# Optimization experiments

Hardware: AMD Instinct MI355X
Metric: run time of the kernel (lower is better)

## Reference

```python
import jax, jax.numpy as jnp
import numpy as np

B, N, D, H, DEPTH = 2, 2048, 768, 12, 4
DH = D // H
SCALE = DH ** -0.5
EPS = 1e-5
FF = 4 * D


def layer_norm(x, w, b):
    m = jnp.mean(x, axis=-1, keepdims=True)
    v = jnp.mean((x - m) ** 2, axis=-1, keepdims=True)
    return (x - m) * jax.lax.rsqrt(v + EPS) * w + b


def to_heads(t):  # [b, n, D] -> [b, H, n, DH]
    b, n, _ = t.shape
    return t.reshape(b, n, H, DH).transpose(0, 2, 1, 3)


def merge_heads(t):  # [b, H, n, DH] -> [b, n, D]
    b, h, n, dh = t.shape
    return t.transpose(0, 2, 1, 3).reshape(b, n, D)


def attend(q, k, v, bias):
    s = jnp.einsum('bhid,bhjd->bhij', q, k) * SCALE + bias
    a = jax.nn.softmax(s, axis=-1)
    return merge_heads(jnp.einsum('bhij,bhjd->bhid', a, v))


def setup_inputs():
    key = jax.random.key(0)
    ks = iter(jax.random.split(key, 16))

    def p(shape, scale=0.02):
        return jax.random.normal(next(ks), shape, dtype=jnp.float32) * scale

    inp = {
        'x': jax.random.normal(next(ks), (B, N, D), dtype=jnp.float32),
        'context': jax.random.normal(next(ks), (B, N, D), dtype=jnp.float32),
        'relative_position_bias': jax.random.normal(next(ks), (1, H, N, N), dtype=jnp.float32) * 0.02,
        # self-attn params (stacked over depth)
        'ln1_w': jnp.ones((DEPTH, D), jnp.float32), 'ln1_b': jnp.zeros((DEPTH, D), jnp.float32),
        'w_qkv': p((DEPTH, D, 3 * D)),
        'w_so': p((DEPTH, D, D)), 'b_so': jnp.zeros((DEPTH, D), jnp.float32),
        # cross-attn params (shared LN applied to x and context, as in source)
        'ln2_w': jnp.ones((DEPTH, D), jnp.float32), 'ln2_b': jnp.zeros((DEPTH, D), jnp.float32),
        'w_q': p((DEPTH, D, D)), 'w_k': p((DEPTH, D, D)), 'w_v': p((DEPTH, D, D)),
        'w_co': p((DEPTH, D, D)), 'b_co': jnp.zeros((DEPTH, D), jnp.float32),
        # FFN params
        'ln3_w': jnp.ones((DEPTH, D), jnp.float32), 'ln3_b': jnp.zeros((DEPTH, D), jnp.float32),
        'w_f1': p((DEPTH, D, FF)), 'b_f1': jnp.zeros((DEPTH, FF), jnp.float32),
        'w_f2': p((DEPTH, FF, D)), 'b_f2': jnp.zeros((DEPTH, D), jnp.float32),
        # final norm
        'lnout_w': jnp.ones((D,), jnp.float32), 'lnout_b': jnp.zeros((D,), jnp.float32),
    }
    return inp


def reference(x, context, relative_position_bias,
              ln1_w, ln1_b, w_qkv, w_so, b_so,
              ln2_w, ln2_b, w_q, w_k, w_v, w_co, b_co,
              ln3_w, ln3_b, w_f1, b_f1, w_f2, b_f2,
              lnout_w, lnout_b):
    bias = relative_position_bias
    for i in range(DEPTH):
        # self-attention block (pre-norm, residual)
        xn = layer_norm(x, ln1_w[i], ln1_b[i])
        q, k, v = jnp.split(xn @ w_qkv[i], 3, axis=-1)
        o = attend(to_heads(q), to_heads(k), to_heads(v), bias)
        x = o @ w_so[i] + b_so[i] + x
        # cross-attention block (input_norm shared for x and context)
        xn = layer_norm(x, ln2_w[i], ln2_b[i])
        cn = layer_norm(context, ln2_w[i], ln2_b[i])
        o = attend(to_heads(xn @ w_q[i]), to_heads(cn @ w_k[i]), to_heads(cn @ w_v[i]), bias)
        x = o @ w_co[i] + b_co[i] + x
        # FFN block
        xn = layer_norm(x, ln3_w[i], ln3_b[i])
        h = jax.nn.gelu(xn @ w_f1[i] + b_f1[i], approximate=False)
        x = h @ w_f2[i] + b_f2[i] + x
    return layer_norm(x, lnout_w, lnout_b)
```

## Files before the change

kernel.cpp:

```cpp
#include <hip/hip_runtime.h>
#include <cstdint>
#include <cstddef>

#define DEV static __device__ __forceinline__

typedef float  f32x4 __attribute__((ext_vector_type(4)));
typedef float  f32x2 __attribute__((ext_vector_type(2)));
typedef short  s16x8 __attribute__((ext_vector_type(8)));
typedef unsigned short u16;
typedef unsigned int   u32;
typedef unsigned int   u32x4 __attribute__((ext_vector_type(4)));
typedef unsigned short u16x2 __attribute__((ext_vector_type(2)));
typedef unsigned short u16x4 __attribute__((ext_vector_type(4)));
typedef __bf16 bf16x8 __attribute__((ext_vector_type(8)));

#define LOG2E 1.4426950408889634f
#define QSCALE_CONST 0.18033688011112042f
#define BSCALE 256.0f
#define BINV   0.00390625f

DEV u16 f2bf(float f){ return __builtin_bit_cast(u16, (__bf16)f); }

DEV float fexp2(float x){
#if __has_builtin(__builtin_amdgcn_exp2f)
  return __builtin_amdgcn_exp2f(x);
#else
  return exp2f(x);
#endif
}

DEV f32x4 mfma16(s16x8 a, s16x8 b, f32x4 c){
  return __builtin_amdgcn_mfma_f32_16x16x32_bf16(
      __builtin_bit_cast(bf16x8, a), __builtin_bit_cast(bf16x8, b), c, 0, 0, 0);
}

DEV void gld16(const void* g, void* l){
  __builtin_amdgcn_global_load_lds(
      (const __attribute__((address_space(1))) void*)(uintptr_t)g,
      (__attribute__((address_space(3))) void*)(unsigned)(uintptr_t)l,
      16, 0, 0);
}

#if __has_builtin(__builtin_amdgcn_cvt_pk_fp8_f32) && __has_builtin(__builtin_amdgcn_cvt_pk_f32_fp8)
DEV u32 pk4_fp8(f32x4 v){
  int r = __builtin_amdgcn_cvt_pk_fp8_f32(v[0], v[1], 0, false);
  r     = __builtin_amdgcn_cvt_pk_fp8_f32(v[2], v[3], r, true);
  return (u32)r;
}
template<bool HI>
DEV f32x2 upk_fp8(u32 w){
  return __builtin_amdgcn_cvt_pk_f32_fp8((int)w, HI);
}
#else
DEV unsigned enc1(float x){
  union{float f; unsigned u;} c; c.f = x;
  unsigned s = (c.u >> 24) & 0x80;
  int e = (int)((c.u >> 23) & 0xff) - 127;
  unsigned m = c.u & 0x7fffff;
  if (e >= -6){
    unsigned mant = m >> 20, rem = m & 0xfffff;
    if (rem > 0x80000 || (rem == 0x80000 && (mant & 1))) mant++;
    unsigned eb = (unsigned)(e + 7);
    if (mant == 8){ mant = 0; eb++; }
    if (eb >= 16){ eb = 15; mant = 6; }
    return s | (eb << 3) | mant;
  }
  if (e < -10) return s;
  int sh = -6 - e;
  unsigned full = (1u << 23) | m;
  unsigned mant = full >> (20 + sh);
  unsigned rem  = full & ((1u << (20 + sh)) - 1);
  unsigned half = 1u << (19 + sh);
  if (rem > half || (rem == half && (mant & 1))) mant++;
  if (mant == 8) return s | (1u << 3);
  return s | mant;
}
DEV u32 pk4_fp8(f32x4 v){
  return enc1(v[0]) | (enc1(v[1]) << 8) | (enc1(v[2]) << 16) | (enc1(v[3]) << 24);
}
DEV float dec1(unsigned b){
  int s = (b >> 7) & 1, e = (b >> 3) & 15; float m = (float)(b & 7) * 0.125f;
  float v = e ? ldexpf(1.0f + m, e - 7) : ldexpf(m, -6);
  return s ? -v : v;
}
template<bool HI>
DEV f32x2 upk_fp8(u32 w){
  unsigned lo = HI ? ((w >> 16) & 0xff) : (w & 0xff);
  unsigned h2 = HI ? ((w >> 24) & 0xff) : ((w >> 8) & 0xff);
  f32x2 r; r[0] = dec1(lo); r[1] = dec1(h2); return r;
}
#endif

__global__ void __launch_bounds__(256)
transpose_cvt(const float* __restrict__ src, u16* __restrict__ dst, int K, int N,
              size_t dzstride){
  int z = blockIdx.z;
  src += (size_t)z * K * N;
  dst += (size_t)z * dzstride;
  __shared__ float t[32][33];
  int n0 = blockIdx.x * 32, k0 = blockIdx.y * 32;
#pragma unroll
  for (int i = 0; i < 4; ++i)
    t[threadIdx.y + 8*i][threadIdx.x] = src[(size_t)(k0 + threadIdx.y + 8*i) * N + n0 + threadIdx.x];
  __syncthreads();
#pragma unroll
  for (int i = 0; i < 4; ++i)
    dst[(size_t)(n0 + threadIdx.y + 8*i) * K + k0 + threadIdx.x] = f2bf(t[threadIdx.x][threadIdx.y + 8*i]);
}

__global__ void __launch_bounds__(256)
cvt_biasT(const float* __restrict__ in, unsigned char* __restrict__ out){
  const int kvt = blockIdx.x, qt = blockIdx.y, h = blockIdx.z, tid = threadIdx.x;
  const int q  = qt * 64 + ((tid >> 6) << 4) + (tid & 15);
  const int c0 = kvt * 64 + ((tid >> 4) & 3) * 4;
  const float* src = in + ((size_t)h * 2048 + q) * 2048;
  u32x4 wv;
#pragma unroll
  for (int mi = 0; mi < 4; ++mi){
    f32x4 v = *(const f32x4*)(src + c0 + mi * 16);
#pragma unroll
    for (int r = 0; r < 4; ++r) v[r] = fminf(fmaxf(v[r] * (LOG2E * BSCALE), -448.f), 448.f);
    wv[mi] = pk4_fp8(v);
  }
  *(u32x4*)(out + ((size_t)(h * 32 + qt) * 32 + kvt) * 4096 + tid * 16) = wv;
}

__global__ void __launch_bounds__(256)
lnv(const float* __restrict__ x, const float* __restrict__ w, const float* __restrict__ b,
    u16* __restrict__ out){
  const int wv = threadIdx.x >> 6, lane = threadIdx.x & 63;
  const float* wz = w + blockIdx.y * 768;
  const float* bz = b + blockIdx.y * 768;
  out += (size_t)blockIdx.y * 4096 * 768;
  const int row = blockIdx.x * 4 + wv;
  const float* xr = x + (size_t)row * 768;
  f32x4 t[3]; float s = 0.f, s2 = 0.f;
#pragma unroll
  for (int c = 0; c < 3; ++c){
    t[c] = *(const f32x4*)(xr + c * 256 + lane * 4);
#pragma unroll
    for (int j = 0; j < 4; ++j){ s += t[c][j]; s2 += t[c][j] * t[c][j]; }
  }
#pragma unroll
  for (int off = 1; off < 64; off <<= 1){ s += __shfl_xor(s, off); s2 += __shfl_xor(s2, off); }
  float m = s * (1.f/768.f);
  float rstd = rsqrtf(s2 * (1.f/768.f) - m * m + 1e-5f);
#pragma unroll
  for (int c = 0; c < 3; ++c){
    const int col = c * 256 + lane * 4;
    f32x4 wv4 = *(const f32x4*)(wz + col);
    f32x4 bv4 = *(const f32x4*)(bz + col);
    u16x4 o;
#pragma unroll
    for (int j = 0; j < 4; ++j) o[j] = f2bf((t[c][j] - m) * rstd * wv4[j] + bv4[j]);
    *(u16x4*)(out + (size_t)row * 768 + col) = o;
  }
}

template<typename OUT>
__global__ void __launch_bounds__(256)
red_ln(const float* __restrict__ p, const float* __restrict__ biasrow,
       float* __restrict__ xbuf, OUT* __restrict__ out,
       const float* __restrict__ lw, const float* __restrict__ lb){
  const int wv = threadIdx.x >> 6, lane = threadIdx.x & 63;
  const int row = blockIdx.x * 4 + wv;
  const size_t S = 4096ll * 768;
  const float* p0 = p + (size_t)row * 768;
  float* xr = xbuf + (size_t)row * 768;
  f32x4 t[3]; float s = 0.f, s2 = 0.f;
#pragma unroll
  for (int c = 0; c < 3; ++c){
    const int col = c * 256 + lane * 4;
    f32x4 v = *(const f32x4*)(p0 + col);
    v += *(const f32x4*)(p0 + S + col);
    v += *(const f32x4*)(p0 + 2*S + col);
    v += *(const f32x4*)(p0 + 3*S + col);
    v += *(const f32x4*)(biasrow + col);
    v += *(const f32x4*)(xr + col);
    *(f32x4*)(xr + col) = v;
    t[c] = v;
#pragma unroll
    for (int j = 0; j < 4; ++j){ s += v[j]; s2 += v[j] * v[j]; }
  }
#pragma unroll
  for (int off = 1; off < 64; off <<= 1){ s += __shfl_xor(s, off); s2 += __shfl_xor(s2, off); }
  float m = s * (1.f/768.f);
  float rstd = rsqrtf(s2 * (1.f/768.f) - m * m + 1e-5f);
#pragma unroll
  for (int c = 0; c < 3; ++c){
    const int col = c * 256 + lane * 4;
    f32x4 wv4 = *(const f32x4*)(lw + col);
    f32x4 bv4 = *(const f32x4*)(lb + col);
    if constexpr (sizeof(OUT) == 2){
      u16x4 o;
#pragma unroll
      for (int j = 0; j < 4; ++j) o[j] = f2bf((t[c][j] - m) * rstd * wv4[j] + bv4[j]);
      *(u16x4*)((u16*)out + (size_t)row * 768 + col) = o;
    } else {
      f32x4 o;
#pragma unroll
      for (int j = 0; j < 4; ++j) o[j] = (t[c][j] - m) * rstd * wv4[j] + bv4[j];
      *(f32x4*)((float*)out + (size_t)row * 768 + col) = o;
    }
  }
}

template<int EPI>
__global__ void __launch_bounds__(256)
gemm_bf16(const u16* __restrict__ A, int lda, const u16* __restrict__ Bt, int ldb,
          int nk, u16* __restrict__ Cb, float* __restrict__ Cf, int ldc,
          const float* __restrict__ bias,
          const u16* __restrict__ A2, const u16* __restrict__ Bt2){
  __shared__ u16 As[2][128 * 32];
  __shared__ u16 Bs[2][128 * 32];
  float colscale = 1.0f;
  if constexpr (EPI == 4){
    const int z = blockIdx.z;
    if (z == 0){ colscale = QSCALE_CONST; }
    else { A = A2; Bt = Bt2 + (size_t)(z - 1) * 768 * 768; }
    Cb += z * 768;
  }
  if constexpr (EPI == 5){
    const int z = blockIdx.z;
    A  += (size_t)z * nk * 32;
    Bt += (size_t)z * nk * 32;
    Cf += (size_t)z * 4096 * 768;
  }
  const int tid = threadIdx.x, w = tid >> 6, lane = tid & 63;
  const int l16 = lane & 15, g = lane >> 4;
  const int m0 = blockIdx.x * 128, n0 = blockIdx.y * 128;
  const int wm = (w >> 1) * 64, wn = (w & 1) * 64;
  f32x4 acc[4][4] = {};

  const u16* a0 = A  + (size_t)(m0 + (tid >> 2)) * lda + (tid & 3) * 8;
  const u16* a1 = A  + (size_t)(m0 + (tid >> 2) + 64) * lda + (tid & 3) * 8;
  const u16* b0 = Bt + (size_t)(n0 + (tid >> 2)) * ldb + (tid & 3) * 8;
  const u16* b1 = Bt + (size_t)(n0 + (tid >> 2) + 64) * ldb + (tid & 3) * 8;

  {
    char* ab = (char*)As[0]; char* bb = (char*)Bs[0];
    gld16(a0, ab + w * 1024); gld16(a1, ab + 4096 + w * 1024);
    gld16(b0, bb + w * 1024); gld16(b1, bb + 4096 + w * 1024);
  }
  __syncthreads();

  int cb = 0;
  for (int kt = 0; kt < nk; ++kt){
    if (kt + 1 < nk){
      const int k1 = (kt + 1) * 32;
      char* ab = (char*)As[cb ^ 1]; char* bb = (char*)Bs[cb ^ 1];
      gld16(a0 + k1, ab + w * 1024); gld16(a1 + k1, ab + 4096 + w * 1024);
      gld16(b0 + k1, bb + w * 1024); gld16(b1 + k1, bb + 4096 + w * 1024);
    }
    const u16* Ab = As[cb]; const u16* Bb = Bs[cb];
    s16x8 af[4], bfv[4];
#pragma unroll
    for (int mi = 0; mi < 4; ++mi)
      af[mi] = *(const s16x8*)(Ab + (wm + mi*16 + l16) * 32 + 8 * g);
#pragma unroll
    for (int ni = 0; ni < 4; ++ni)
      bfv[ni] = *(const s16x8*)(Bb + (wn + ni*16 + l16) * 32 + 8 * g);
#pragma unroll
    for (int mi = 0; mi < 4; ++mi)
#pragma unroll
      for (int ni = 0; ni < 4; ++ni)
        acc[mi][ni] = mfma16(af[mi], bfv[ni], acc[mi][ni]);
    __syncthreads();
    cb ^= 1;
  }

#pragma unroll
  for (int mi = 0; mi < 4; ++mi){
    const int rg = m0 + wm + mi*16 + 4*g;
#pragma unroll
    for (int ni = 0; ni < 4; ++ni){
      const int col = n0 + wn + ni*16 + l16;
      f32x4 v = acc[mi][ni];
#pragma unroll
      for (int r = 0; r < 4; ++r){
        const int row = rg + r;
        if constexpr (EPI == 2){
          float t = v[r] + bias[col];
          float ge = 0.5f * t * (1.0f + erff(t * 0.7071067811865476f));
          Cb[(size_t)row * ldc + col] = f2bf(ge);
        } else if constexpr (EPI == 3){
          float sc = (col < 768) ? QSCALE_CONST : 1.0f;
          Cb[(size_t)row * ldc + col] = f2bf(v[r] * sc);
        } else if constexpr (EPI == 4){
          Cb[(size_t)row * ldc + col] = f2bf(v[r] * colscale);
        } else {
          Cf[(size_t)row * 768 + col] = v[r];
        }
      }
    }
  }
}

__global__ void __launch_bounds__(256)
attn_kernel(const u16* __restrict__ qkv, const unsigned char* __restrict__ biasT,
            u16* __restrict__ out){
  __shared__ __align__(16) u16 Ks[2][4096];
  __shared__ __align__(16) u16 Vt[2][4096];
  __shared__ __align__(16) u16 Pl[4][1024];

  const int tid = threadIdx.x, w = tid >> 6, lane = tid & 63;
  const int l16 = lane & 15, g = lane >> 4;
  const int qt = blockIdx.x, h = blockIdx.y, b = blockIdx.z;
  const int rowbase = b * 2048, q0 = qt * 64;

  const int ci0 = w * 64 + lane, ci1 = ci0 + 256;
  const int r0 = ci0 >> 3, sc0 = ci0 & 7, r1 = ci1 >> 3, sc1 = ci1 & 7;
  const u16* kp0 = qkv + (size_t)(rowbase + r0) * 2304 + 768 + h * 64 + (((sc0 ^ (r0 & 7)) & 7) << 3);
  const u16* kp1 = qkv + (size_t)(rowbase + r1) * 2304 + 768 + h * 64 + (((sc1 ^ (r1 & 7)) & 7) << 3);
  const int dh0 = (tid & 31) * 2, vs = tid >> 5;
  const u16* vp = qkv + (size_t)(rowbase + vs * 8) * 2304 + 1536 + h * 64 + dh0;
  u16x2 vr[8];
  const unsigned char* bT = biasT + ((size_t)(h * 32 + qt) * 32) * 4096 + tid * 16;
  u32x4 brW, bnW;

  const u16* qrow = qkv + (size_t)(rowbase + q0 + w * 16 + l16) * 2304 + h * 64;
  s16x8 qf0 = *(const s16x8*)(qrow + 8 * g);
  s16x8 qf1 = *(const s16x8*)(qrow + 32 + 8 * g);

  f32x4 oacc[4] = {};
  float mrun = -3.0e38f, lrun = 0.f;
  const int sw = l16 & 7;

  {
    char* kb = (char*)Ks[0] + w * 1024;
    gld16(kp0, kb); gld16(kp1, kb + 4096);
#pragma unroll
    for (int i = 0; i < 8; ++i) vr[i] = *(const u16x2*)(vp + (size_t)i * 2304);
    brW = *(const u32x4*)(bT);
    s16x8 vA, vB;
#pragma unroll
    for (int j = 0; j < 8; ++j){ vA[j] = (short)vr[j][0]; vB[j] = (short)vr[j][1]; }
    *(s16x8*)(Vt[0] + dh0 * 64 + ((vs ^ (dh0 & 7)) << 3)) = vA;
    *(s16x8*)(Vt[0] + (dh0 + 1) * 64 + ((vs ^ ((dh0 + 1) & 7)) << 3)) = vB;
  }
  __syncthreads();

  for (int t = 0; t < 32; ++t){
    const int cb = t & 1;
    if (t < 31){
      const size_t koff = (size_t)(t + 1) * 64 * 2304;
      char* kb = (char*)Ks[cb ^ 1] + w * 1024;
      gld16(kp0 + koff, kb); gld16(kp1 + koff, kb + 4096);
      const u16* p = vp + koff;
#pragma unroll
      for (int i = 0; i < 8; ++i) vr[i] = *(const u16x2*)(p + (size_t)i * 2304);
      bnW = *(const u32x4*)(bT + (size_t)(t + 1) * 4096);
    }

    f32x4 st[4];
    __builtin_amdgcn_s_setprio(1);
#pragma unroll
    for (int mi = 0; mi < 4; ++mi){
      const int row = l16 + 16 * mi;
      s16x8 kf0 = *(const s16x8*)(Ks[cb] + row * 64 + ((g ^ sw) << 3));
      s16x8 kf1 = *(const s16x8*)(Ks[cb] + row * 64 + (((g + 4) ^ sw) << 3));
      f32x4 z = {};
      z = mfma16(kf0, qf0, z);
      st[mi] = mfma16(kf1, qf1, z);
    }
    __builtin_amdgcn_s_setprio(0);

    float tmax = -3.0e38f;
#pragma unroll
    for (int mi = 0; mi < 4; ++mi){
      f32x2 lo = upk_fp8<false>(brW[mi]);
      f32x2 hi = upk_fp8<true>(brW[mi]);
      st[mi][0] = fmaf(lo[0], BINV, st[mi][0]);
      st[mi][1] = fmaf(lo[1], BINV, st[mi][1]);
      st[mi][2] = fmaf(hi[0], BINV, st[mi][2]);
      st[mi][3] = fmaf(hi[1], BINV, st[mi][3]);
#pragma unroll
      for (int r = 0; r < 4; ++r) tmax = fmaxf(tmax, st[mi][r]);
    }
    tmax = fmaxf(tmax, __shfl_xor(tmax, 16));
    tmax = fmaxf(tmax, __shfl_xor(tmax, 32));
    if (!__all(tmax <= mrun + 8.f)){
      float mnew = fmaxf(mrun, tmax);
      float al = fexp2(mrun - mnew);
      mrun = mnew;
      lrun *= al;
#pragma unroll
      for (int r = 0; r < 4; ++r){
        float aq = __shfl(al, 4 * g + r);
#pragma unroll
        for (int ni = 0; ni < 4; ++ni) oacc[ni][r] *= aq;
      }
    }
    float ssum = 0.f;
#pragma unroll
    for (int mi = 0; mi < 4; ++mi){
      u16x4 pk;
#pragma unroll
      for (int r = 0; r < 4; ++r){
        float pv = fexp2(st[mi][r] - mrun);
        ssum += pv;
        pk[r] = f2bf(pv);
      }
      *(u16x4*)(Pl[w] + l16 * 64 + (((2*mi + (g >> 1)) ^ sw) << 3) + 4 * (g & 1)) = pk;
    }
    ssum += __shfl_xor(ssum, 16);
    ssum += __shfl_xor(ssum, 32);
    lrun += ssum;

    __builtin_amdgcn_s_setprio(1);
#pragma unroll
    for (int ks2 = 0; ks2 < 2; ++ks2){
      s16x8 pf = *(const s16x8*)(Pl[w] + l16 * 64 + (((4*ks2 + g) ^ sw) << 3));
#pragma unroll
      for (int ni = 0; ni < 4; ++ni){
        const int dh = l16 + 16 * ni;
        s16x8 vf = *(const s16x8*)(Vt[cb] + dh * 64 + (((4*ks2 + g) ^ sw) << 3));
        oacc[ni] = mfma16(pf, vf, oacc[ni]);
      }
    }
    __builtin_amdgcn_s_setprio(0);

    if (t < 31){
      s16x8 vA, vB;
#pragma unroll
      for (int j = 0; j < 8; ++j){ vA[j] = (short)vr[j][0]; vB[j] = (short)vr[j][1]; }
      *(s16x8*)(Vt[cb ^ 1] + dh0 * 64 + ((vs ^ (dh0 & 7)) << 3)) = vA;
      *(s16x8*)(Vt[cb ^ 1] + (dh0 + 1) * 64 + ((vs ^ ((dh0 + 1) & 7)) << 3)) = vB;
      brW = bnW;
    }
    __syncthreads();
  }

#pragma unroll
  for (int r = 0; r < 4; ++r){
    float lq = __shfl(lrun, 4 * g + r);
    float inv = 1.0f / lq;
    const int row = rowbase + q0 + w * 16 + 4 * g + r;
#pragma unroll
    for (int ni = 0; ni < 4; ++ni)
      out[(size_t)row * 768 + h * 64 + l16 + 16 * ni] = f2bf(oacc[ni][r] * inv);
  }
}

extern "C" void kernel_launch(void* const* d_in, const int* in_sizes, int n_in,
                              void* d_out, int out_size, void* d_ws, size_t ws_size,
                              hipStream_t stream){
  const float* in_x    = (const float*)d_in[0];
  const float* in_ctx  = (const float*)d_in[1];
  const float* in_bias = (const float*)d_in[2];
  const float* ln1_w = (const float*)d_in[3];
  const float* ln1_b = (const float*)d_in[4];
  const float* w_qkv = (const float*)d_in[5];
  const float* w_so  = (const float*)d_in[6];
  const float* b_so  = (const float*)d_in[7];
  const float* ln2_w = (const float*)d_in[8];
  const float* ln2_b = (const float*)d_in[9];
  const float* w_q   = (const float*)d_in[10];
  const float* w_k   = (const float*)d_in[11];
  const float* w_v   = (const float*)d_in[12];
  const float* w_co  = (const float*)d_in[13];
  const float* b_co  = (const float*)d_in[14];
  const float* ln3_w = (const float*)d_in[15];
  const float* ln3_b = (const float*)d_in[16];
  const float* w_f1  = (const float*)d_in[17];
  const float* b_f1  = (const float*)d_in[18];
  const float* w_f2  = (const float*)d_in[19];
  const float* b_f2  = (const float*)d_in[20];
  const float* lnout_w = (const float*)d_in[21];
  const float* lnout_b = (const float*)d_in[22];

  char* p = (char*)d_ws;
  float* xbuf  = (float*)p;  p += 4096ll * 768 * 4;
  float* pbuf  = (float*)p;  p += 4ll * 4096 * 768 * 4;
  u16* xn      = (u16*)p;    p += 4096ll * 768 * 2;
  u16* cn      = (u16*)p;    p += 4ll * 4096 * 768 * 2;
  u16* qkvb    = (u16*)p;    p += 4096ll * 2304 * 2;
  u16* attO    = (u16*)p;    p += 4096ll * 768 * 2;
  u16* ffh     = (u16*)p;    p += 4096ll * 3072 * 2;
  u16* wqkvT   = (u16*)p;    p += 4ll * 2304 * 768 * 2;
  u16* wsoT    = (u16*)p;    p += 4ll * 768 * 768 * 2;
  u16* wqT     = (u16*)p;    p += 4ll * 768 * 768 * 2;
  u16* wkvT    = (u16*)p;    p += 4ll * 1536 * 768 * 2;
  u16* wcoT    = (u16*)p;    p += 4ll * 768 * 768 * 2;
  u16* wf1T    = (u16*)p;    p += 4ll * 3072 * 768 * 2;
  u16* wf2T    = (u16*)p;    p += 4ll * 768 * 3072 * 2;
  unsigned char* biasT = (unsigned char*)p; p += 12ll * 2048 * 2048;

  hipMemcpyAsync(xbuf, in_x, 4096ll * 768 * 4, hipMemcpyDeviceToDevice, stream);

  const dim3 tb(32, 8);
  transpose_cvt<<<dim3(72, 24, 4), tb, 0, stream>>>(w_qkv, wqkvT, 768, 2304, 2304ll*768);
  transpose_cvt<<<dim3(24, 24, 4), tb, 0, stream>>>(w_so,  wsoT,  768, 768,  768ll*768);
  transpose_cvt<<<dim3(24, 24, 4), tb, 0, stream>>>(w_q,   wqT,   768, 768,  768ll*768);
  transpose_cvt<<<dim3(24, 24, 4), tb, 0, stream>>>(w_k,   wkvT,             768, 768, 1536ll*768);
  transpose_cvt<<<dim3(24, 24, 4), tb, 0, stream>>>(w_v,   wkvT + 768ll*768, 768, 768, 1536ll*768);
  transpose_cvt<<<dim3(24, 24, 4), tb, 0, stream>>>(w_co,  wcoT,  768, 768,  768ll*768);
  transpose_cvt<<<dim3(96, 24, 4), tb, 0, stream>>>(w_f1,  wf1T,  768, 3072, 3072ll*768);
  transpose_cvt<<<dim3(24, 96, 4), tb, 0, stream>>>(w_f2,  wf2T,  3072, 768, 768ll*3072);
  cvt_biasT<<<dim3(32, 32, 12), 256, 0, stream>>>(in_bias, biasT);
  lnv<<<dim3(1024, 4), 256, 0, stream>>>(in_ctx, ln2_w, ln2_b, cn);
  lnv<<<dim3(1024, 1), 256, 0, stream>>>(xbuf, ln1_w, ln1_b, xn);

  const dim3 ag(32, 12, 2);
  for (int i = 0; i < 4; ++i){
    gemm_bf16<3><<<dim3(32, 18), 256, 0, stream>>>(xn, 768, wqkvT + (size_t)i*2304*768, 768, 24,
                                                   qkvb, nullptr, 2304, nullptr, nullptr, nullptr);
    attn_kernel<<<ag, 256, 0, stream>>>(qkvb, biasT, attO);
    gemm_bf16<5><<<dim3(32, 6, 4), 256, 0, stream>>>(attO, 768, wsoT + (size_t)i*768*768, 768, 6,
                                                     nullptr, pbuf, 768, nullptr, nullptr, nullptr);
    red_ln<u16><<<1024, 256, 0, stream>>>(pbuf, b_so + i*768, xbuf, xn, ln2_w + i*768, ln2_b + i*768);
    gemm_bf16<4><<<dim3(32, 6, 3), 256, 0, stream>>>(xn, 768, wqT + (size_t)i*768*768, 768, 24,
                                                     qkvb, nullptr, 2304, nullptr,
                                                     cn + (size_t)i*4096*768, wkvT + (size_t)i*1536*768);
    attn_kernel<<<ag, 256, 0, stream>>>(qkvb, biasT, attO);
    gemm_bf16<5><<<dim3(32, 6, 4), 256, 0, stream>>>(attO, 768, wcoT + (size_t)i*768*768, 768, 6,
                                                     nullptr, pbuf, 768, nullptr, nullptr, nullptr);
    red_ln<u16><<<1024, 256, 0, stream>>>(pbuf, b_co + i*768, xbuf, xn, ln3_w + i*768, ln3_b + i*768);
    gemm_bf16<2><<<dim3(32, 24), 256, 0, stream>>>(xn, 768, wf1T + (size_t)i*3072*768, 768, 24,
                                                   ffh, nullptr, 3072, b_f1 + i*3072, nullptr, nullptr);
    gemm_bf16<5><<<dim3(32, 6, 4), 256, 0, stream>>>(ffh, 3072, wf2T + (size_t)i*768*3072, 3072, 24,
                                                     nullptr, pbuf, 768, nullptr, nullptr, nullptr);
    if (i < 3)
      red_ln<u16><<<1024, 256, 0, stream>>>(pbuf, b_f2 + i*768, xbuf, xn, ln1_w + (i+1)*768, ln1_b + (i+1)*768);
    else
      red_ln<float><<<1024, 256, 0, stream>>>(pbuf, b_f2 + i*768, xbuf, (float*)d_out, lnout_w, lnout_b);
  }
}
```

Before: 1.355 ms.

## Store split-K partials in bf16, remap GEMM blocks across XCDs, batch weight transposes

```diff
diff --git a/kernel.cpp b/kernel.cpp
--- a/kernel.cpp
+++ b/kernel.cpp
@@ -20,6 +20,7 @@
 #define BINV   0.00390625f
 
 DEV u16 f2bf(float f){ return __builtin_bit_cast(u16, (__bf16)f); }
+DEV float bf2f(u16 v){ union { unsigned u; float f; } x; x.u = ((unsigned)v) << 16; return x.f; }
 
 DEV float fexp2(float x){
 #if __has_builtin(__builtin_amdgcn_exp2f)
@@ -108,6 +109,22 @@
     dst[(size_t)(n0 + threadIdx.y + 8*i) * K + k0 + threadIdx.x] = f2bf(t[threadIdx.x][threadIdx.y + 8*i]);
 }
 
+struct TPtrs { const float* src[20]; u16* dst[20]; };
+__global__ void __launch_bounds__(256)
+transpose_cvt_batch(TPtrs tp){
+  const float* src = tp.src[blockIdx.z];
+  u16* dst = tp.dst[blockIdx.z];
+  __shared__ float t[32][33];
+  int n0 = blockIdx.x * 32, k0 = blockIdx.y * 32;
+#pragma unroll
+  for (int i = 0; i < 4; ++i)
+    t[threadIdx.y + 8*i][threadIdx.x] = src[(size_t)(k0 + threadIdx.y + 8*i) * 768 + n0 + threadIdx.x];
+  __syncthreads();
+#pragma unroll
+  for (int i = 0; i < 4; ++i)
+    dst[(size_t)(n0 + threadIdx.y + 8*i) * 768 + k0 + threadIdx.x] = f2bf(t[threadIdx.x][threadIdx.y + 8*i]);
+}
+
 __global__ void __launch_bounds__(256)
 cvt_biasT(const float* __restrict__ in, unsigned char* __restrict__ out){
   const int kvt = blockIdx.x, qt = blockIdx.y, h = blockIdx.z, tid = threadIdx.x;
@@ -159,24 +176,26 @@
 
 template<typename OUT>
 __global__ void __launch_bounds__(256)
-red_ln(const float* __restrict__ p, const float* __restrict__ biasrow,
+red_ln(const u16* __restrict__ pb, const float* __restrict__ biasrow,
        float* __restrict__ xbuf, OUT* __restrict__ out,
        const float* __restrict__ lw, const float* __restrict__ lb){
   const int wv = threadIdx.x >> 6, lane = threadIdx.x & 63;
   const int row = blockIdx.x * 4 + wv;
   const size_t S = 4096ll * 768;
-  const float* p0 = p + (size_t)row * 768;
+  const u16* p0 = pb + (size_t)row * 768;
   float* xr = xbuf + (size_t)row * 768;
   f32x4 t[3]; float s = 0.f, s2 = 0.f;
 #pragma unroll
   for (int c = 0; c < 3; ++c){
     const int col = c * 256 + lane * 4;
-    f32x4 v = *(const f32x4*)(p0 + col);
-    v += *(const f32x4*)(p0 + S + col);
-    v += *(const f32x4*)(p0 + 2*S + col);
-    v += *(const f32x4*)(p0 + 3*S + col);
-    v += *(const f32x4*)(biasrow + col);
+    f32x4 v = *(const f32x4*)(biasrow + col);
     v += *(const f32x4*)(xr + col);
+#pragma unroll
+    for (int z = 0; z < 4; ++z){
+      u16x4 pv = *(const u16x4*)(p0 + z * S + col);
+#pragma unroll
+      for (int j = 0; j < 4; ++j) v[j] += bf2f(pv[j]);
+    }
     *(f32x4*)(xr + col) = v;
     t[c] = v;
 #pragma unroll
@@ -208,7 +227,7 @@
 template<int EPI>
 __global__ void __launch_bounds__(256)
 gemm_bf16(const u16* __restrict__ A, int lda, const u16* __restrict__ Bt, int ldb,
-          int nk, u16* __restrict__ Cb, float* __restrict__ Cf, int ldc,
+          int nk, u16* __restrict__ Cb, int ldc,
           const float* __restrict__ bias,
           const u16* __restrict__ A2, const u16* __restrict__ Bt2){
   __shared__ u16 As[2][128 * 32];
@@ -224,11 +243,19 @@
     const int z = blockIdx.z;
     A  += (size_t)z * nk * 32;
     Bt += (size_t)z * nk * 32;
-    Cf += (size_t)z * 4096 * 768;
-  }
+    Cb += (size_t)z * 4096 * 768;
+  }
+  const int gx = gridDim.x, nwg = gx * gridDim.y;
+  int lin = blockIdx.y * gx + blockIdx.x;
+  {
+    const int qq = nwg >> 3, rr = nwg & 7;
+    const int xc = lin & 7, oo = lin >> 3;
+    lin = (xc < rr ? xc * (qq + 1) : rr * (qq + 1) + (xc - rr) * qq) + oo;
+  }
+  const int m0 = (lin % gx) * 128, n0 = (lin / gx) * 128;
+
   const int tid = threadIdx.x, w = tid >> 6, lane = tid & 63;
   const int l16 = lane & 15, g = lane >> 4;
-  const int m0 = blockIdx.x * 128, n0 = blockIdx.y * 128;
   const int wm = (w >> 1) * 64, wn = (w & 1) * 64;
   f32x4 acc[4][4] = {};
 
@@ -289,7 +316,7 @@
         } else if constexpr (EPI == 4){
           Cb[(size_t)row * ldc + col] = f2bf(v[r] * colscale);
         } else {
-          Cf[(size_t)row * 768 + col] = v[r];
+          Cb[(size_t)row * 768 + col] = f2bf(v[r]);
         }
       }
     }
@@ -471,7 +498,7 @@
 
   char* p = (char*)d_ws;
   float* xbuf  = (float*)p;  p += 4096ll * 768 * 4;
-  float* pbuf  = (float*)p;  p += 4ll * 4096 * 768 * 4;
+  u16* pbuf    = (u16*)p;    p += 4ll * 4096 * 768 * 2;
   u16* xn      = (u16*)p;    p += 4096ll * 768 * 2;
   u16* cn      = (u16*)p;    p += 4ll * 4096 * 768 * 2;
   u16* qkvb    = (u16*)p;    p += 4096ll * 2304 * 2;
@@ -490,13 +517,19 @@
 
   const dim3 tb(32, 8);
   transpose_cvt<<<dim3(72, 24, 4), tb, 0, stream>>>(w_qkv, wqkvT, 768, 2304, 2304ll*768);
-  transpose_cvt<<<dim3(24, 24, 4), tb, 0, stream>>>(w_so,  wsoT,  768, 768,  768ll*768);
-  transpose_cvt<<<dim3(24, 24, 4), tb, 0, stream>>>(w_q,   wqT,   768, 768,  768ll*768);
-  transpose_cvt<<<dim3(24, 24, 4), tb, 0, stream>>>(w_k,   wkvT,             768, 768, 1536ll*768);
-  transpose_cvt<<<dim3(24, 24, 4), tb, 0, stream>>>(w_v,   wkvT + 768ll*768, 768, 768, 1536ll*768);
-  transpose_cvt<<<dim3(24, 24, 4), tb, 0, stream>>>(w_co,  wcoT,  768, 768,  768ll*768);
   transpose_cvt<<<dim3(96, 24, 4), tb, 0, stream>>>(w_f1,  wf1T,  768, 3072, 3072ll*768);
   transpose_cvt<<<dim3(24, 96, 4), tb, 0, stream>>>(w_f2,  wf2T,  3072, 768, 768ll*3072);
+  {
+    TPtrs tp;
+    for (int i = 0; i < 4; ++i){
+      tp.src[i*5+0] = w_so + (size_t)i*768*768;  tp.dst[i*5+0] = wsoT + (size_t)i*768*768;
+      tp.src[i*5+1] = w_q  + (size_t)i*768*768;  tp.dst[i*5+1] = wqT  + (size_t)i*768*768;
+      tp.src[i*5+2] = w_k  + (size_t)i*768*768;  tp.dst[i*5+2] = wkvT + (size_t)i*1536*768;
+      tp.src[i*5+3] = w_v  + (size_t)i*768*768;  tp.dst[i*5+3] = wkvT + (size_t)i*1536*768 + 768ll*768;
+      tp.src[i*5+4] = w_co + (size_t)i*768*768;  tp.dst[i*5+4] = wcoT + (size_t)i*768*768;
+    }
+    transpose_cvt_batch<<<dim3(24, 24, 20), tb, 0, stream>>>(tp);
+  }
   cvt_biasT<<<dim3(32, 32, 12), 256, 0, stream>>>(in_bias, biasT);
   lnv<<<dim3(1024, 4), 256, 0, stream>>>(in_ctx, ln2_w, ln2_b, cn);
   lnv<<<dim3(1024, 1), 256, 0, stream>>>(xbuf, ln1_w, ln1_b, xn);
@@ -504,22 +537,22 @@
   const dim3 ag(32, 12, 2);
   for (int i = 0; i < 4; ++i){
     gemm_bf16<3><<<dim3(32, 18), 256, 0, stream>>>(xn, 768, wqkvT + (size_t)i*2304*768, 768, 24,
-                                                   qkvb, nullptr, 2304, nullptr, nullptr, nullptr);
+                                                   qkvb, 2304, nullptr, nullptr, nullptr);
     attn_kernel<<<ag, 256, 0, stream>>>(qkvb, biasT, attO);
     gemm_bf16<5><<<dim3(32, 6, 4), 256, 0, stream>>>(attO, 768, wsoT + (size_t)i*768*768, 768, 6,
-                                                     nullptr, pbuf, 768, nullptr, nullptr, nullptr);
+                                                     pbuf, 768, nullptr, nullptr, nullptr);
     red_ln<u16><<<1024, 256, 0, stream>>>(pbuf, b_so + i*768, xbuf, xn, ln2_w + i*768, ln2_b + i*768);
     gemm_bf16<4><<<dim3(32, 6, 3), 256, 0, stream>>>(xn, 768, wqT + (size_t)i*768*768, 768, 24,
-                                                     qkvb, nullptr, 2304, nullptr,
+                                                     qkvb, 2304, nullptr,
                                                      cn + (size_t)i*4096*768, wkvT + (size_t)i*1536*768);
     attn_kernel<<<ag, 256, 0, stream>>>(qkvb, biasT, attO);
     gemm_bf16<5><<<dim3(32, 6, 4), 256, 0, stream>>>(attO, 768, wcoT + (size_t)i*768*768, 768, 6,
-                                                     nullptr, pbuf, 768, nullptr, nullptr, nullptr);
+                                                     pbuf, 768, nullptr, nullptr, nullptr);
     red_ln<u16><<<1024, 256, 0, stream>>>(pbuf, b_co + i*768, xbuf, xn, ln3_w + i*768, ln3_b + i*768);
     gemm_bf16<2><<<dim3(32, 24), 256, 0, stream>>>(xn, 768, wf1T + (size_t)i*3072*768, 768, 24,
-                                                   ffh, nullptr, 3072, b_f1 + i*3072, nullptr, nullptr);
+                                                   ffh, 3072, b_f1 + i*3072, nullptr, nullptr);
     gemm_bf16<5><<<dim3(32, 6, 4), 256, 0, stream>>>(ffh, 3072, wf2T + (size_t)i*768*3072, 3072, 24,
-                                                     nullptr, pbuf, 768, nullptr, nullptr, nullptr);
+                                                     pbuf, 768, nullptr, nullptr, nullptr);
     if (i < 3)
       red_ln<u16><<<1024, 256, 0, stream>>>(pbuf, b_f2 + i*768, xbuf, xn, ln1_w + (i+1)*768, ln1_b + (i+1)*768);
     else
```

Result: faster. 1.313 ms (-3.1%).
